# Kernel optimization log

Hardware: AMD Instinct MI355X
Metric: run time of the kernel (lower is better)

The kernel has to match this reference:

```python
import jax, jax.numpy as jnp
import numpy as np


def setup_inputs() -> dict:
    key = jax.random.key(0)
    k1, k2, k3 = jax.random.split(key, 3)
    B, S, E = 4, 4096, 512
    x = jax.random.normal(k1, (B, S, E), dtype=jnp.float32)
    # xavier_uniform for Linear weights; zero biases (per _reset_parameters)
    lim_qkv = float(np.sqrt(6.0 / (E + 3 * E)))
    W_qkv = jax.random.uniform(k2, (3 * E, E), minval=-lim_qkv, maxval=lim_qkv, dtype=jnp.float32)
    b_qkv = jnp.zeros((3 * E,), dtype=jnp.float32)
    lim_out = float(np.sqrt(6.0 / (E + E)))
    W_out = jax.random.uniform(k3, (E, E), minval=-lim_out, maxval=lim_out, dtype=jnp.float32)
    b_out = jnp.zeros((E,), dtype=jnp.float32)
    return {"x": x, "W_qkv": W_qkv, "b_qkv": b_qkv, "W_out": W_out, "b_out": b_out}


def reference(x, W_qkv, b_qkv, W_out, b_out):
    B, S, E = x.shape
    H = 8
    D = E // H
    qkv = x @ W_qkv.T + b_qkv                      # [B,S,3E]
    qkv = qkv.reshape(B, S, H, 3 * D)
    q, k, v = jnp.split(qkv, 3, axis=-1)            # each [B,S,H,D]
    q = jax.nn.sigmoid(q)
    k = jax.nn.sigmoid(k)
    # flow conservation normalizers (sum over seq dim=1, then feature dim=3)
    i = jnp.sum(q * jnp.sum(k, axis=1, keepdims=True), axis=3, keepdims=True)      # [B,S,H,1]
    o = jnp.sum(k * jnp.sum(q, axis=1, keepdims=True), axis=3, keepdims=True)
    i_hat = jnp.sum(q * jnp.sum(k / o, axis=1, keepdims=True), axis=3, keepdims=True)
    o_hat = jnp.sum(k * jnp.sum(q / i, axis=1, keepdims=True), axis=3, keepdims=True)
    # NOTE: faithful to source — matmul batches over (B,S) and contracts the HEAD axis
    vw = v * jax.nn.softmax(o_hat, axis=1)          # [B,S,H,D]
    kv = jnp.einsum('bshd,bshe->bsde', k, vw)       # [B,S,D,D]
    r = jnp.einsum('bshd,bsde->bshe', q / i, kv) * jax.nn.sigmoid(i_hat)  # [B,S,H,D]
    values = r.reshape(B, S, E)
    return values @ W_out.T + b_out
```

## Files before the change

kernel.cpp:

```cpp
#include <hip/hip_runtime.h>
#include <cstdint>
#include <cstddef>

#define B_ 4
#define S_ 4096
#define E_ 512
#define NPOS 16384
#define QKVC 1536
#define K_ 512

typedef unsigned short u16;
typedef u16    u16x8  __attribute__((ext_vector_type(8)));
typedef u16    u16x4  __attribute__((ext_vector_type(4)));
typedef __bf16 bf16x8 __attribute__((ext_vector_type(8)));
typedef float  f32x4  __attribute__((ext_vector_type(4)));

__device__ __forceinline__ u16 f2bf(float f) {
    unsigned u = __builtin_bit_cast(unsigned, f);
    unsigned r = (u + 0x7fffu + ((u >> 16) & 1u)) >> 16;
    return (u16)r;
}
__device__ __forceinline__ float bf2f(u16 u) {
    return __builtin_bit_cast(float, (unsigned)u << 16);
}
__device__ __forceinline__ float rcpf(float x) { return __builtin_amdgcn_rcpf(x); }

__device__ __forceinline__ void async16(const void* g, void* lds) {
    __builtin_amdgcn_global_load_lds(
        (const __attribute__((address_space(1))) unsigned int*)g,
        (__attribute__((address_space(3))) unsigned int*)lds, 16, 0, 0);
}

__global__ void cvt_kernel(const float4* __restrict__ in, u16x4* __restrict__ out, int n4) {
    int i = blockIdx.x * 256 + threadIdx.x;
    if (i < n4) {
        float4 v = in[i];
        u16x4 o;
        o[0] = f2bf(v.x); o[1] = f2bf(v.y); o[2] = f2bf(v.z); o[3] = f2bf(v.w);
        out[i] = o;
    }
}

__device__ __forceinline__ void mfma_step(const u16* AsB, const u16* BsB,
                                          int wm, int wn, int fr, int fkk,
                                          f32x4 (&acc)[4][4]) {
    bf16x8 a[4], b[4];
    #pragma unroll
    for (int i = 0; i < 4; ++i)
        a[i] = *(const bf16x8*)&AsB[(wm + i * 16 + fr) * 32 + fkk];
    #pragma unroll
    for (int j = 0; j < 4; ++j)
        b[j] = *(const bf16x8*)&BsB[(wn + j * 16 + fr) * 32 + fkk];
    __builtin_amdgcn_s_setprio(1);
    #pragma unroll
    for (int i = 0; i < 4; ++i)
        #pragma unroll
        for (int j = 0; j < 4; ++j)
            acc[i][j] = __builtin_amdgcn_mfma_f32_16x16x32_bf16(a[i], b[j], acc[i][j], 0, 0, 0);
    __builtin_amdgcn_s_setprio(0);
}

#define GEMM_PIPELINE(NT)                                                     \
    {                                                                          \
        STAGE(0, 0);                                                           \
        STAGE(1, 1);                                                           \
        asm volatile("s_waitcnt vmcnt(4)" ::: "memory");                       \
        __builtin_amdgcn_s_barrier();                                          \
        __builtin_amdgcn_sched_barrier(0);                                     \
        int cb = 0, sb = 1;                                                    \
        for (int t = 0; t < (NT) - 2; ++t) {                                   \
            sb = (sb == 2) ? 0 : sb + 1;                                       \
            STAGE(t + 2, sb);                                                  \
            mfma_step(As[cb], Bs[cb], wm, wn, fr, fkk, acc);                   \
            asm volatile("s_waitcnt vmcnt(4)" ::: "memory");                   \
            __builtin_amdgcn_s_barrier();                                      \
            __builtin_amdgcn_sched_barrier(0);                                 \
            cb = (cb == 2) ? 0 : cb + 1;                                       \
        }                                                                      \
        mfma_step(As[cb], Bs[cb], wm, wn, fr, fkk, acc);                       \
        asm volatile("s_waitcnt vmcnt(0)" ::: "memory");                       \
        __builtin_amdgcn_s_barrier();                                          \
        __builtin_amdgcn_sched_barrier(0);                                     \
        cb = (cb == 2) ? 0 : cb + 1;                                           \
        mfma_step(As[cb], Bs[cb], wm, wn, fr, fkk, acc);                       \
    }

__global__ __launch_bounds__(256) void gemm_qkv(
        const u16* __restrict__ A, const u16* __restrict__ Bw,
        const float* __restrict__ bias,
        u16* __restrict__ Qb, u16* __restrict__ Kb, u16* __restrict__ Vb,
        float* __restrict__ sumq, float* __restrict__ sumk,
        int K) {
    __shared__ u16 As[3][128 * 32];
    __shared__ u16 Bs[3][128 * 32];
    const int tid  = threadIdx.x;
    const int wave = tid >> 6, lane = tid & 63;
    const int bid = blockIdx.x;
    const int swz = (bid & 7) * 192 + (bid >> 3);
    const int m0 = (swz / 12) * 128, n0 = (swz % 12) * 128;
    const int wm = (wave & 1) * 64, wn = (wave >> 1) * 64;

    const int srow = wave * 16 + (lane >> 2);
    const int cgs  = (lane & 3) ^ ((lane >> 2) & 3) ^ ((lane >> 4) & 3);
    const u16* Ap = A  + (size_t)(m0 + srow) * K + cgs * 8;
    const u16* Bp = Bw + (size_t)(n0 + srow) * K + cgs * 8;
    const int woff = wave * 512;
    const size_t rstep = (size_t)64 * K;

    f32x4 acc[4][4] = {};
    const int fr  = lane & 15;
    const int fkk = (((lane >> 4) ^ (fr & 3) ^ ((fr >> 2) & 3))) * 8;

    #define STAGE(t, buf)                                             \
        async16(Ap + (t) * 32,         &As[buf][woff]);               \
        async16(Ap + (t) * 32 + rstep, &As[buf][woff + 2048]);        \
        async16(Bp + (t) * 32,         &Bs[buf][woff]);               \
        async16(Bp + (t) * 32 + rstep, &Bs[buf][woff + 2048]);

    const int nt = K >> 5;
    GEMM_PIPELINE(nt)
    #undef STAGE

    const int cn = lane & 15, rb = (lane >> 4) * 4;
    const int cg   = (n0 + wn) >> 6;
    const int type = cg % 3;
    const int hb   = cg / 3;
    u16* dst = (type == 0) ? Qb : (type == 1) ? Kb : Vb;
    const bool sg = (type < 2);
    float colsum[4] = {};
    #pragma unroll
    for (int i = 0; i < 4; ++i) {
        int mbase = m0 + wm + i * 16 + rb;
        #pragma unroll
        for (int j = 0; j < 4; ++j) {
            int ccol = j * 16 + cn;
            float bv = bias[n0 + wn + ccol];
            int outcol = hb * 64 + ccol;
            f32x4 av = acc[i][j];
            #pragma unroll
            for (int r = 0; r < 4; ++r) {
                float v = av[r] + bv;
                if (sg) { v = 1.f / (1.f + __expf(-v)); colsum[j] += v; }
                dst[(size_t)(mbase + r) * 512 + outcol] = f2bf(v);
            }
        }
    }
    if (sg) {
        float* sdst = (type == 0) ? sumq : sumk;
        const int b = m0 >> 12;
        #pragma unroll
        for (int j = 0; j < 4; ++j) {
            float s = colsum[j];
            s += __shfl_xor(s, 16);
            s += __shfl_xor(s, 32);
            if (lane < 16)
                atomicAdd(&sdst[b * 512 + hb * 64 + j * 16 + cn], s);
        }
    }
}

__global__ __launch_bounds__(256) void gemm_out(
        const u16* __restrict__ A, const u16* __restrict__ Bw,
        const float* __restrict__ bias, float* __restrict__ C,
        int N, int K) {
    __shared__ u16 As[3][128 * 32];
    __shared__ u16 Bs[3][128 * 32];
    const int tid  = threadIdx.x;
    const int wave = tid >> 6, lane = tid & 63;
    const int bid = blockIdx.x;
    const int swz = (bid & 7) * 64 + (bid >> 3);
    const int m0 = (swz >> 2) * 128, n0 = (swz & 3) * 128;
    const int wm = (wave & 1) * 64, wn = (wave >> 1) * 64;
    const int srow = wave * 16 + (lane >> 2);
    const int cgs  = (lane & 3) ^ ((lane >> 2) & 3) ^ ((lane >> 4) & 3);
    const u16* Ap = A  + (size_t)(m0 + srow) * K + cgs * 8;
    const u16* Bp = Bw + (size_t)(n0 + srow) * K + cgs * 8;
    const int woff = wave * 512;
    const size_t rstep = (size_t)64 * K;
    f32x4 acc[4][4] = {};
    const int fr  = lane & 15;
    const int fkk = (((lane >> 4) ^ (fr & 3) ^ ((fr >> 2) & 3))) * 8;

    #define STAGE(t, buf)                                             \
        async16(Ap + (t) * 32,         &As[buf][woff]);               \
        async16(Ap + (t) * 32 + rstep, &As[buf][woff + 2048]);        \
        async16(Bp + (t) * 32,         &Bs[buf][woff]);               \
        async16(Bp + (t) * 32 + rstep, &Bs[buf][woff + 2048]);

    const int nt = K >> 5;
    GEMM_PIPELINE(nt)
    #undef STAGE

    const int cn = lane & 15, rb = (lane >> 4) * 4;
    #pragma unroll
    for (int i = 0; i < 4; ++i) {
        int mbase = m0 + wm + i * 16 + rb;
        #pragma unroll
        for (int j = 0; j < 4; ++j) {
            int nn = n0 + wn + j * 16 + cn;
            float bv = bias[nn];
            f32x4 av = acc[i][j];
            #pragma unroll
            for (int r = 0; r < 4; ++r)
                C[(size_t)(mbase + r) * N + nn] = av[r] + bv;
        }
    }
}

__global__ __launch_bounds__(256) void fused_io(const u16* __restrict__ Qg, const u16* __restrict__ Kg,
                                                const float* __restrict__ sumq, const float* __restrict__ sumk,
                                                float* __restrict__ iv,
                                                float* __restrict__ sumqi, float* __restrict__ sumko) {
    int b = blockIdx.x, sc = blockIdx.y;
    int w = threadIdx.x >> 6, lane = threadIdx.x & 63;
    float skL[8], sqL[8];
    #pragma unroll
    for (int j = 0; j < 8; ++j) {
        skL[j] = sumk[b * 512 + lane * 8 + j];
        sqL[j] = sumq[b * 512 + lane * 8 + j];
    }
    float aqi[8] = {}, ako[8] = {};
    int p0 = b * S_ + sc * 32 + w * 8;
    for (int it = 0; it < 8; ++it) {
        int p = p0 + it;
        size_t off = (size_t)p * 512 + lane * 8;
        u16x8 q8 = *(const u16x8*)(Qg + off);
        u16x8 k8 = *(const u16x8*)(Kg + off);
        float qf[8], kf[8];
        #pragma unroll
        for (int j = 0; j < 8; ++j) { qf[j] = bf2f(q8[j]); kf[j] = bf2f(k8[j]); }
        float di = 0.f, dox = 0.f;
        #pragma unroll
        for (int j = 0; j < 8; ++j) { di += qf[j] * skL[j]; dox += kf[j] * sqL[j]; }
        di  += __shfl_xor(di, 1);  di  += __shfl_xor(di, 2);  di  += __shfl_xor(di, 4);
        dox += __shfl_xor(dox, 1); dox += __shfl_xor(dox, 2); dox += __shfl_xor(dox, 4);
        if ((lane & 7) == 0) iv[(size_t)p * 8 + (lane >> 3)] = di;
        float ri = rcpf(di), ro = rcpf(dox);
        #pragma unroll
        for (int j = 0; j < 8; ++j) { aqi[j] += qf[j] * ri; ako[j] += kf[j] * ro; }
    }
    __shared__ float red[4][1024];
    #pragma unroll
    for (int j = 0; j < 8; ++j) {
        red[w][lane * 8 + j]       = aqi[j];
        red[w][512 + lane * 8 + j] = ako[j];
    }
    __syncthreads();
    int t = threadIdx.x;
    #pragma unroll
    for (int rr = 0; rr < 4; ++rr) {
        int slot = rr * 256 + t;
        float s = red[0][slot] + red[1][slot] + red[2][slot] + red[3][slot];
        float* dst = (slot < 512) ? &sumqi[b * 512 + slot] : &sumko[b * 512 + (slot - 512)];
        atomicAdd(dst, s);
    }
}

__global__ __launch_bounds__(256) void io2_kernel(const u16* __restrict__ Qg, const u16* __restrict__ Kg,
                                                  const float* __restrict__ sumqi, const float* __restrict__ sumko,
                                                  const float* __restrict__ iv,
                                                  float* __restrict__ rowsc, float* __restrict__ wexp,
                                                  float* __restrict__ sm) {
    int b = blockIdx.x, sc = blockIdx.y;
    int w = threadIdx.x >> 6, lane = threadIdx.x & 63;
    float skoL[8], sqiL[8];
    #pragma unroll
    for (int j = 0; j < 8; ++j) {
        skoL[j] = sumko[b * 512 + lane * 8 + j];
        sqiL[j] = sumqi[b * 512 + lane * 8 + j];
    }
    float smacc = 0.f;
    int p0 = b * S_ + sc * 32 + w * 8;
    for (int it = 0; it < 8; ++it) {
        int p = p0 + it;
        size_t off = (size_t)p * 512 + lane * 8;
        u16x8 q8 = *(const u16x8*)(Qg + off);
        u16x8 k8 = *(const u16x8*)(Kg + off);
        float dih = 0.f, doh = 0.f;
        #pragma unroll
        for (int j = 0; j < 8; ++j) {
            dih += bf2f(q8[j]) * skoL[j];
            doh += bf2f(k8[j]) * sqiL[j];
        }
        dih += __shfl_xor(dih, 1); dih += __shfl_xor(dih, 2); dih += __shfl_xor(dih, 4);
        doh += __shfl_xor(doh, 1); doh += __shfl_xor(doh, 2); doh += __shfl_xor(doh, 4);
        if ((lane & 7) == 0) {
            int h = lane >> 3;
            float sig = 1.f / (1.f + __expf(-dih));
            rowsc[(size_t)p * 8 + h] = sig * rcpf(iv[(size_t)p * 8 + h]);
            float we = __expf(fminf(doh, 80.f));
            wexp[(size_t)p * 8 + h] = we;
            smacc += we;
        }
    }
    __shared__ float sr[4][8];
    if ((lane & 7) == 0) sr[w][lane >> 3] = smacc;
    __syncthreads();
    if (threadIdx.x < 8)
        atomicAdd(&sm[b * 8 + threadIdx.x],
                  sr[0][threadIdx.x] + sr[1][threadIdx.x] + sr[2][threadIdx.x] + sr[3][threadIdx.x]);
}

__global__ __launch_bounds__(256) void finalize_kernel(
        const u16* __restrict__ Qg, const u16* __restrict__ Kg, const u16* __restrict__ Vg,
        const float* __restrict__ rowsc, const float* __restrict__ wexp, const float* __restrict__ sm,
        u16* __restrict__ Rg) {
    __shared__ float Ml[4][2][8][9];
    __shared__ float vw[4][2][8][68];
    int w = threadIdx.x >> 6, lane = threadIdx.x & 63;
    int p0 = (blockIdx.x * 4 + w) * 2;
    int b = p0 >> 12;

    {
        int pl = (lane >> 3) & 1, hh = lane & 7, quad = lane >> 4;
        const u16* qa = Qg + (size_t)(p0 + pl) * 512 + hh * 64 + quad * 8;
        const u16* ka = Kg + (size_t)(p0 + pl) * 512 + hh * 64 + quad * 8;
        bf16x8 a0 = __builtin_bit_cast(bf16x8, *(const u16x8*)qa);
        bf16x8 a1 = __builtin_bit_cast(bf16x8, *(const u16x8*)(qa + 32));
        bf16x8 b0 = __builtin_bit_cast(bf16x8, *(const u16x8*)ka);
        bf16x8 b1 = __builtin_bit_cast(bf16x8, *(const u16x8*)(ka + 32));
        f32x4 accm = {0.f, 0.f, 0.f, 0.f};
        accm = __builtin_amdgcn_mfma_f32_16x16x32_bf16(a0, b0, accm, 0, 0, 0);
        accm = __builtin_amdgcn_mfma_f32_16x16x32_bf16(a1, b1, accm, 0, 0, 0);
        if (((lane >> 5) & 1) == ((lane >> 3) & 1)) {
            int plm = lane >> 5, hr = ((lane >> 4) & 1) * 4, h2 = lane & 7;
            #pragma unroll
            for (int r = 0; r < 4; ++r) Ml[w][plm][hr + r][h2] = accm[r];
        }
    }
    {
        int hv = lane >> 3, e0 = (lane & 7) * 8;
        float invsm = rcpf(sm[b * 8 + hv]);
        #pragma unroll
        for (int pl = 0; pl < 2; ++pl) {
            u16x8 v8 = *(const u16x8*)(Vg + (size_t)(p0 + pl) * 512 + lane * 8);
            float wgt = wexp[(size_t)(p0 + pl) * 8 + hv] * invsm;
            f32x4 x0, x1;
            #pragma unroll
            for (int j = 0; j < 4; ++j) { x0[j] = bf2f(v8[j]) * wgt; x1[j] = bf2f(v8[4 + j]) * wgt; }
            *(f32x4*)&vw[w][pl][hv][e0]     = x0;
            *(f32x4*)&vw[w][pl][hv][e0 + 4] = x1;
        }
    }
    __syncthreads();
    {
        int pl = lane >> 5, idx = lane & 31, h = idx >> 2, eq = (idx & 3) * 16;
        float out[16] = {};
        #pragma unroll
        for (int h2 = 0; h2 < 8; ++h2) {
            float m = Ml[w][pl][h][h2];
            #pragma unroll
            for (int c = 0; c < 4; ++c) {
                f32x4 vv = *(const f32x4*)&vw[w][pl][h2][eq + c * 4];
                #pragma unroll
                for (int j = 0; j < 4; ++j) out[c * 4 + j] += m * vv[j];
            }
        }
        float rs = rowsc[(size_t)(p0 + pl) * 8 + h];
        u16x8 o0, o1;
        #pragma unroll
        for (int j = 0; j < 8; ++j) { o0[j] = f2bf(out[j] * rs); o1[j] = f2bf(out[8 + j] * rs); }
        u16* dst = Rg + (size_t)(p0 + pl) * 512 + h * 64 + eq;
        *(u16x8*)dst       = o0;
        *(u16x8*)(dst + 8) = o1;
    }
}

extern "C" void kernel_launch(void* const* d_in, const int* in_sizes, int n_in,
                              void* d_out, int out_size, void* d_ws, size_t ws_size,
                              hipStream_t stream) {
    const float* x    = (const float*)d_in[0];
    const float* Wqkv = (const float*)d_in[1];
    const float* bqkv = (const float*)d_in[2];
    const float* Wout = (const float*)d_in[3];
    const float* bout = (const float*)d_in[4];
    float* out = (float*)d_out;
    char* ws = (char*)d_ws;

    constexpr size_t SZ_XBF  = (size_t)NPOS * E_ * 2;
    constexpr size_t SZ_WQBF = (size_t)QKVC * E_ * 2;
    constexpr size_t SZ_WOBF = (size_t)E_ * E_ * 2;
    constexpr size_t SZ_QKVB = (size_t)NPOS * E_ * 2;
    constexpr size_t SZ_SUM  = (size_t)B_ * 512 * 4;
    constexpr size_t SZ_V8   = (size_t)NPOS * 8 * 4;

    size_t off = 0;
    u16*   xbf   = (u16*)(ws + off);   off += SZ_XBF;
    u16*   wqbf  = (u16*)(ws + off);   off += SZ_WQBF;
    u16*   wobf  = (u16*)(ws + off);   off += SZ_WOBF;
    u16*   Qb    = (u16*)(ws + off);   off += SZ_QKVB;
    u16*   Kb    = (u16*)(ws + off);   off += SZ_QKVB;
    u16*   Vb    = (u16*)(ws + off);   off += SZ_QKVB;
    char*  zbase = ws + off;
    float* sumq  = (float*)(ws + off); off += SZ_SUM;
    float* sumk  = (float*)(ws + off); off += SZ_SUM;
    float* sumqi = (float*)(ws + off); off += SZ_SUM;
    float* sumko = (float*)(ws + off); off += SZ_SUM;
    float* sm    = (float*)(ws + off); off += 256;
    size_t zlen  = (char*)(ws + off) - zbase;
    float* iv    = (float*)(ws + off); off += SZ_V8;
    float* rowsc = (float*)(ws + off); off += SZ_V8;
    float* wexp  = (float*)(ws + off); off += SZ_V8;
    u16*   rbf   = xbf;

    hipMemsetAsync(zbase, 0, zlen, stream);

    cvt_kernel<<<(NPOS * E_ / 4) / 256, 256, 0, stream>>>((const float4*)x, (u16x4*)xbf, NPOS * E_ / 4);
    cvt_kernel<<<(QKVC * E_ / 4) / 256, 256, 0, stream>>>((const float4*)Wqkv, (u16x4*)wqbf, QKVC * E_ / 4);
    cvt_kernel<<<(E_ * E_ / 4) / 256, 256, 0, stream>>>((const float4*)Wout, (u16x4*)wobf, E_ * E_ / 4);

    gemm_qkv<<<dim3((QKVC / 128) * (NPOS / 128)), 256, 0, stream>>>(xbf, wqbf, bqkv, Qb, Kb, Vb, sumq, sumk, K_);

    fused_io<<<dim3(B_, 128), 256, 0, stream>>>(Qb, Kb, sumq, sumk, iv, sumqi, sumko);
    io2_kernel<<<dim3(B_, 128), 256, 0, stream>>>(Qb, Kb, sumqi, sumko, iv, rowsc, wexp, sm);
    finalize_kernel<<<NPOS / 8, 256, 0, stream>>>(Qb, Kb, Vb, rowsc, wexp, sm, rbf);

    gemm_out<<<dim3((E_ / 128) * (NPOS / 128)), 256, 0, stream>>>(rbf, wobf, bout, out, E_, K_);
}
```

Measured before the change: 186.3 us.

## Fuse flow-normalizer kernels into one cooperative kernel with LDS-resident Q/K

```diff
diff --git a/kernel.cpp b/kernel.cpp
--- a/kernel.cpp
+++ b/kernel.cpp
@@ -1,6 +1,9 @@
 #include <hip/hip_runtime.h>
+#include <hip/hip_cooperative_groups.h>
 #include <cstdint>
 #include <cstddef>
+
+namespace cg = cooperative_groups;
 
 #define B_ 4
 #define S_ 4096
@@ -31,14 +34,21 @@
         (__attribute__((address_space(3))) unsigned int*)lds, 16, 0, 0);
 }
 
-__global__ void cvt_kernel(const float4* __restrict__ in, u16x4* __restrict__ out, int n4) {
+#define CVT_N1 (NPOS * E_ / 4)
+#define CVT_N2 (QKVC * E_ / 4)
+#define CVT_N3 (E_ * E_ / 4)
+__global__ void cvt_all(const float4* __restrict__ x,  u16x4* __restrict__ xo,
+                        const float4* __restrict__ wq, u16x4* __restrict__ wqo,
+                        const float4* __restrict__ wo, u16x4* __restrict__ woo) {
     int i = blockIdx.x * 256 + threadIdx.x;
-    if (i < n4) {
-        float4 v = in[i];
-        u16x4 o;
-        o[0] = f2bf(v.x); o[1] = f2bf(v.y); o[2] = f2bf(v.z); o[3] = f2bf(v.w);
-        out[i] = o;
-    }
+    const float4* in; u16x4* out; int idx;
+    if (i < CVT_N1)                { in = x;  out = xo;  idx = i; }
+    else if (i < CVT_N1 + CVT_N2)  { in = wq; out = wqo; idx = i - CVT_N1; }
+    else                           { in = wo; out = woo; idx = i - CVT_N1 - CVT_N2; }
+    float4 v = in[idx];
+    u16x4 o;
+    o[0] = f2bf(v.x); o[1] = f2bf(v.y); o[2] = f2bf(v.z); o[3] = f2bf(v.w);
+    out[idx] = o;
 }
 
 __device__ __forceinline__ void mfma_step(const u16* AsB, const u16* BsB,
@@ -122,9 +132,9 @@
     #undef STAGE
 
     const int cn = lane & 15, rb = (lane >> 4) * 4;
-    const int cg   = (n0 + wn) >> 6;
-    const int type = cg % 3;
-    const int hb   = cg / 3;
+    const int cg2  = (n0 + wn) >> 6;
+    const int type = cg2 % 3;
+    const int hb   = cg2 / 3;
     u16* dst = (type == 0) ? Qb : (type == 1) ? Kb : Vb;
     const bool sg = (type < 2);
     float colsum[4] = {};
@@ -207,162 +217,178 @@
     }
 }
 
-__global__ __launch_bounds__(256) void fused_io(const u16* __restrict__ Qg, const u16* __restrict__ Kg,
-                                                const float* __restrict__ sumq, const float* __restrict__ sumk,
-                                                float* __restrict__ iv,
-                                                float* __restrict__ sumqi, float* __restrict__ sumko) {
-    int b = blockIdx.x, sc = blockIdx.y;
-    int w = threadIdx.x >> 6, lane = threadIdx.x & 63;
-    float skL[8], sqL[8];
-    #pragma unroll
-    for (int j = 0; j < 8; ++j) {
-        skL[j] = sumk[b * 512 + lane * 8 + j];
-        sqL[j] = sumq[b * 512 + lane * 8 + j];
-    }
-    float aqi[8] = {}, ako[8] = {};
-    int p0 = b * S_ + sc * 32 + w * 8;
-    for (int it = 0; it < 8; ++it) {
-        int p = p0 + it;
-        size_t off = (size_t)p * 512 + lane * 8;
-        u16x8 q8 = *(const u16x8*)(Qg + off);
-        u16x8 k8 = *(const u16x8*)(Kg + off);
-        float qf[8], kf[8];
-        #pragma unroll
-        for (int j = 0; j < 8; ++j) { qf[j] = bf2f(q8[j]); kf[j] = bf2f(k8[j]); }
-        float di = 0.f, dox = 0.f;
-        #pragma unroll
-        for (int j = 0; j < 8; ++j) { di += qf[j] * skL[j]; dox += kf[j] * sqL[j]; }
-        di  += __shfl_xor(di, 1);  di  += __shfl_xor(di, 2);  di  += __shfl_xor(di, 4);
-        dox += __shfl_xor(dox, 1); dox += __shfl_xor(dox, 2); dox += __shfl_xor(dox, 4);
-        if ((lane & 7) == 0) iv[(size_t)p * 8 + (lane >> 3)] = di;
-        float ri = rcpf(di), ro = rcpf(dox);
-        #pragma unroll
-        for (int j = 0; j < 8; ++j) { aqi[j] += qf[j] * ri; ako[j] += kf[j] * ro; }
-    }
-    __shared__ float red[4][1024];
-    #pragma unroll
-    for (int j = 0; j < 8; ++j) {
-        red[w][lane * 8 + j]       = aqi[j];
-        red[w][512 + lane * 8 + j] = ako[j];
-    }
-    __syncthreads();
-    int t = threadIdx.x;
-    #pragma unroll
-    for (int rr = 0; rr < 4; ++rr) {
-        int slot = rr * 256 + t;
-        float s = red[0][slot] + red[1][slot] + red[2][slot] + red[3][slot];
-        float* dst = (slot < 512) ? &sumqi[b * 512 + slot] : &sumko[b * 512 + (slot - 512)];
-        atomicAdd(dst, s);
-    }
-}
-
-__global__ __launch_bounds__(256) void io2_kernel(const u16* __restrict__ Qg, const u16* __restrict__ Kg,
-                                                  const float* __restrict__ sumqi, const float* __restrict__ sumko,
-                                                  const float* __restrict__ iv,
-                                                  float* __restrict__ rowsc, float* __restrict__ wexp,
-                                                  float* __restrict__ sm) {
-    int b = blockIdx.x, sc = blockIdx.y;
-    int w = threadIdx.x >> 6, lane = threadIdx.x & 63;
-    float skoL[8], sqiL[8];
-    #pragma unroll
-    for (int j = 0; j < 8; ++j) {
-        skoL[j] = sumko[b * 512 + lane * 8 + j];
-        sqiL[j] = sumqi[b * 512 + lane * 8 + j];
-    }
-    float smacc = 0.f;
-    int p0 = b * S_ + sc * 32 + w * 8;
-    for (int it = 0; it < 8; ++it) {
-        int p = p0 + it;
-        size_t off = (size_t)p * 512 + lane * 8;
-        u16x8 q8 = *(const u16x8*)(Qg + off);
-        u16x8 k8 = *(const u16x8*)(Kg + off);
-        float dih = 0.f, doh = 0.f;
+__global__ __launch_bounds__(256) void coopflow(
+        const u16* __restrict__ Qg, const u16* __restrict__ Kg, const u16* __restrict__ Vg,
+        const float* __restrict__ sumq, const float* __restrict__ sumk,
+        float* __restrict__ sumqi, float* __restrict__ sumko, float* __restrict__ sm,
+        u16* __restrict__ Rg) {
+    __shared__ u16 Qs[64 * 512];
+    __shared__ u16 Ks[64 * 512];
+    __shared__ float scratch[4928];
+    __shared__ float iv_l[64][8];
+    __shared__ float rowsc_l[64][8];
+    __shared__ float wexp_l[64][8];
+    __shared__ float sr[4][8];
+
+    const int bid = blockIdx.x;
+    const int b   = bid >> 6;
+    const int P0  = b * S_ + (bid & 63) * 64;
+    const int w = threadIdx.x >> 6, lane = threadIdx.x & 63;
+
+    {
+        float* red = scratch;
+        float skL[8], sqL[8];
         #pragma unroll
         for (int j = 0; j < 8; ++j) {
-            dih += bf2f(q8[j]) * skoL[j];
-            doh += bf2f(k8[j]) * sqiL[j];
-        }
-        dih += __shfl_xor(dih, 1); dih += __shfl_xor(dih, 2); dih += __shfl_xor(dih, 4);
-        doh += __shfl_xor(doh, 1); doh += __shfl_xor(doh, 2); doh += __shfl_xor(doh, 4);
-        if ((lane & 7) == 0) {
-            int h = lane >> 3;
-            float sig = 1.f / (1.f + __expf(-dih));
-            rowsc[(size_t)p * 8 + h] = sig * rcpf(iv[(size_t)p * 8 + h]);
-            float we = __expf(fminf(doh, 80.f));
-            wexp[(size_t)p * 8 + h] = we;
-            smacc += we;
-        }
-    }
-    __shared__ float sr[4][8];
-    if ((lane & 7) == 0) sr[w][lane >> 3] = smacc;
-    __syncthreads();
-    if (threadIdx.x < 8)
-        atomicAdd(&sm[b * 8 + threadIdx.x],
-                  sr[0][threadIdx.x] + sr[1][threadIdx.x] + sr[2][threadIdx.x] + sr[3][threadIdx.x]);
-}
-
-__global__ __launch_bounds__(256) void finalize_kernel(
-        const u16* __restrict__ Qg, const u16* __restrict__ Kg, const u16* __restrict__ Vg,
-        const float* __restrict__ rowsc, const float* __restrict__ wexp, const float* __restrict__ sm,
-        u16* __restrict__ Rg) {
-    __shared__ float Ml[4][2][8][9];
-    __shared__ float vw[4][2][8][68];
-    int w = threadIdx.x >> 6, lane = threadIdx.x & 63;
-    int p0 = (blockIdx.x * 4 + w) * 2;
-    int b = p0 >> 12;
+            skL[j] = sumk[b * 512 + lane * 8 + j];
+            sqL[j] = sumq[b * 512 + lane * 8 + j];
+        }
+        for (int half = 0; half < 2; ++half) {
+            float aqi[8] = {}, ako[8] = {};
+            int pl0 = half * 32 + w * 8;
+            for (int it = 0; it < 8; ++it) {
+                int pll = pl0 + it;
+                size_t off = (size_t)(P0 + pll) * 512 + lane * 8;
+                u16x8 q8 = *(const u16x8*)(Qg + off);
+                u16x8 k8 = *(const u16x8*)(Kg + off);
+                *(u16x8*)&Qs[pll * 512 + lane * 8] = q8;
+                *(u16x8*)&Ks[pll * 512 + lane * 8] = k8;
+                float qf[8], kf[8];
+                #pragma unroll
+                for (int j = 0; j < 8; ++j) { qf[j] = bf2f(q8[j]); kf[j] = bf2f(k8[j]); }
+                float di = 0.f, dox = 0.f;
+                #pragma unroll
+                for (int j = 0; j < 8; ++j) { di += qf[j] * skL[j]; dox += kf[j] * sqL[j]; }
+                di  += __shfl_xor(di, 1);  di  += __shfl_xor(di, 2);  di  += __shfl_xor(di, 4);
+                dox += __shfl_xor(dox, 1); dox += __shfl_xor(dox, 2); dox += __shfl_xor(dox, 4);
+                if ((lane & 7) == 0) iv_l[pll][lane >> 3] = di;
+                float ri = rcpf(di), ro = rcpf(dox);
+                #pragma unroll
+                for (int j = 0; j < 8; ++j) { aqi[j] += qf[j] * ri; ako[j] += kf[j] * ro; }
+            }
+            #pragma unroll
+            for (int j = 0; j < 8; ++j) {
+                red[w * 1024 + lane * 8 + j]       = aqi[j];
+                red[w * 1024 + 512 + lane * 8 + j] = ako[j];
+            }
+            __syncthreads();
+            int t = threadIdx.x;
+            #pragma unroll
+            for (int rr = 0; rr < 4; ++rr) {
+                int slot = rr * 256 + t;
+                float s = red[slot] + red[1024 + slot] + red[2048 + slot] + red[3072 + slot];
+                float* dst = (slot < 512) ? &sumqi[b * 512 + slot] : &sumko[b * 512 + (slot - 512)];
+                atomicAdd(dst, s);
+            }
+            __syncthreads();
+        }
+    }
+    cg::this_grid().sync();
 
     {
-        int pl = (lane >> 3) & 1, hh = lane & 7, quad = lane >> 4;
-        const u16* qa = Qg + (size_t)(p0 + pl) * 512 + hh * 64 + quad * 8;
-        const u16* ka = Kg + (size_t)(p0 + pl) * 512 + hh * 64 + quad * 8;
-        bf16x8 a0 = __builtin_bit_cast(bf16x8, *(const u16x8*)qa);
-        bf16x8 a1 = __builtin_bit_cast(bf16x8, *(const u16x8*)(qa + 32));
-        bf16x8 b0 = __builtin_bit_cast(bf16x8, *(const u16x8*)ka);
-        bf16x8 b1 = __builtin_bit_cast(bf16x8, *(const u16x8*)(ka + 32));
-        f32x4 accm = {0.f, 0.f, 0.f, 0.f};
-        accm = __builtin_amdgcn_mfma_f32_16x16x32_bf16(a0, b0, accm, 0, 0, 0);
-        accm = __builtin_amdgcn_mfma_f32_16x16x32_bf16(a1, b1, accm, 0, 0, 0);
-        if (((lane >> 5) & 1) == ((lane >> 3) & 1)) {
-            int plm = lane >> 5, hr = ((lane >> 4) & 1) * 4, h2 = lane & 7;
-            #pragma unroll
-            for (int r = 0; r < 4; ++r) Ml[w][plm][hr + r][h2] = accm[r];
-        }
-    }
+        float skoL[8], sqiL[8];
+        #pragma unroll
+        for (int j = 0; j < 8; ++j) {
+            skoL[j] = sumko[b * 512 + lane * 8 + j];
+            sqiL[j] = sumqi[b * 512 + lane * 8 + j];
+        }
+        for (int half = 0; half < 2; ++half) {
+            float smacc = 0.f;
+            int pl0 = half * 32 + w * 8;
+            for (int it = 0; it < 8; ++it) {
+                int pll = pl0 + it;
+                u16x8 q8 = *(const u16x8*)&Qs[pll * 512 + lane * 8];
+                u16x8 k8 = *(const u16x8*)&Ks[pll * 512 + lane * 8];
+                float dih = 0.f, doh = 0.f;
+                #pragma unroll
+                for (int j = 0; j < 8; ++j) {
+                    dih += bf2f(q8[j]) * skoL[j];
+                    doh += bf2f(k8[j]) * sqiL[j];
+                }
+                dih += __shfl_xor(dih, 1); dih += __shfl_xor(dih, 2); dih += __shfl_xor(dih, 4);
+                doh += __shfl_xor(doh, 1); doh += __shfl_xor(doh, 2); doh += __shfl_xor(doh, 4);
+                if ((lane & 7) == 0) {
+                    int h = lane >> 3;
+                    float sig = 1.f / (1.f + __expf(-dih));
+                    rowsc_l[pll][h] = sig * rcpf(iv_l[pll][h]);
+                    float we = __expf(fminf(doh, 80.f));
+                    wexp_l[pll][h] = we;
+                    smacc += we;
+                }
+            }
+            if ((lane & 7) == 0) sr[w][lane >> 3] = smacc;
+            __syncthreads();
+            if (threadIdx.x < 8)
+                atomicAdd(&sm[b * 8 + threadIdx.x],
+                          sr[0][threadIdx.x] + sr[1][threadIdx.x] + sr[2][threadIdx.x] + sr[3][threadIdx.x]);
+            __syncthreads();
+        }
+    }
+    cg::this_grid().sync();
+
     {
-        int hv = lane >> 3, e0 = (lane & 7) * 8;
-        float invsm = rcpf(sm[b * 8 + hv]);
-        #pragma unroll
-        for (int pl = 0; pl < 2; ++pl) {
-            u16x8 v8 = *(const u16x8*)(Vg + (size_t)(p0 + pl) * 512 + lane * 8);
-            float wgt = wexp[(size_t)(p0 + pl) * 8 + hv] * invsm;
-            f32x4 x0, x1;
-            #pragma unroll
-            for (int j = 0; j < 4; ++j) { x0[j] = bf2f(v8[j]) * wgt; x1[j] = bf2f(v8[4 + j]) * wgt; }
-            *(f32x4*)&vw[w][pl][hv][e0]     = x0;
-            *(f32x4*)&vw[w][pl][hv][e0 + 4] = x1;
-        }
-    }
-    __syncthreads();
-    {
-        int pl = lane >> 5, idx = lane & 31, h = idx >> 2, eq = (idx & 3) * 16;
-        float out[16] = {};
-        #pragma unroll
-        for (int h2 = 0; h2 < 8; ++h2) {
-            float m = Ml[w][pl][h][h2];
-            #pragma unroll
-            for (int c = 0; c < 4; ++c) {
-                f32x4 vv = *(const f32x4*)&vw[w][pl][h2][eq + c * 4];
-                #pragma unroll
-                for (int j = 0; j < 4; ++j) out[c * 4 + j] += m * vv[j];
-            }
-        }
-        float rs = rowsc[(size_t)(p0 + pl) * 8 + h];
-        u16x8 o0, o1;
-        #pragma unroll
-        for (int j = 0; j < 8; ++j) { o0[j] = f2bf(out[j] * rs); o1[j] = f2bf(out[8 + j] * rs); }
-        u16* dst = Rg + (size_t)(p0 + pl) * 512 + h * 64 + eq;
-        *(u16x8*)dst       = o0;
-        *(u16x8*)(dst + 8) = o1;
+        float* Ml = scratch;
+        float* vw = scratch + 576;
+        const float invsm = rcpf(sm[b * 8 + (lane >> 3)]);
+        __syncthreads();
+        for (int g = 0; g < 8; ++g) {
+            const int ploc = g * 8 + w * 2;
+            const int p0g  = P0 + ploc;
+            {
+                int pl = (lane >> 3) & 1, hh = lane & 7, quad = lane >> 4;
+                const u16* qa = &Qs[(ploc + pl) * 512 + hh * 64 + quad * 8];
+                const u16* ka = &Ks[(ploc + pl) * 512 + hh * 64 + quad * 8];
+                bf16x8 a0 = __builtin_bit_cast(bf16x8, *(const u16x8*)qa);
+                bf16x8 a1 = __builtin_bit_cast(bf16x8, *(const u16x8*)(qa + 32));
+                bf16x8 b0 = __builtin_bit_cast(bf16x8, *(const u16x8*)ka);
+                bf16x8 b1 = __builtin_bit_cast(bf16x8, *(const u16x8*)(ka + 32));
+                f32x4 accm = {0.f, 0.f, 0.f, 0.f};
+                accm = __builtin_amdgcn_mfma_f32_16x16x32_bf16(a0, b0, accm, 0, 0, 0);
+                accm = __builtin_amdgcn_mfma_f32_16x16x32_bf16(a1, b1, accm, 0, 0, 0);
+                if (((lane >> 5) & 1) == ((lane >> 3) & 1)) {
+                    int plm = lane >> 5, hr = ((lane >> 4) & 1) * 4, h2 = lane & 7;
+                    #pragma unroll
+                    for (int r = 0; r < 4; ++r)
+                        Ml[w * 144 + plm * 72 + (hr + r) * 9 + h2] = accm[r];
+                }
+            }
+            {
+                int hv = lane >> 3, e0 = (lane & 7) * 8;
+                #pragma unroll
+                for (int pl = 0; pl < 2; ++pl) {
+                    u16x8 v8 = *(const u16x8*)(Vg + (size_t)(p0g + pl) * 512 + lane * 8);
+                    float wgt = wexp_l[ploc + pl][hv] * invsm;
+                    f32x4 x0, x1;
+                    #pragma unroll
+                    for (int j = 0; j < 4; ++j) { x0[j] = bf2f(v8[j]) * wgt; x1[j] = bf2f(v8[4 + j]) * wgt; }
+                    *(f32x4*)&vw[w * 1088 + pl * 544 + hv * 68 + e0]     = x0;
+                    *(f32x4*)&vw[w * 1088 + pl * 544 + hv * 68 + e0 + 4] = x1;
+                }
+            }
+            __syncthreads();
+            {
+                int pl = lane >> 5, idx = lane & 31, h = idx >> 2, eq = (idx & 3) * 16;
+                float out[16] = {};
+                #pragma unroll
+                for (int h2 = 0; h2 < 8; ++h2) {
+                    float m = Ml[w * 144 + pl * 72 + h * 9 + h2];
+                    #pragma unroll
+                    for (int c = 0; c < 4; ++c) {
+                        f32x4 vv = *(const f32x4*)&vw[w * 1088 + pl * 544 + h2 * 68 + eq + c * 4];
+                        #pragma unroll
+                        for (int j = 0; j < 4; ++j) out[c * 4 + j] += m * vv[j];
+                    }
+                }
+                float rs = rowsc_l[ploc + pl][h];
+                u16x8 o0, o1;
+                #pragma unroll
+                for (int j = 0; j < 8; ++j) { o0[j] = f2bf(out[j] * rs); o1[j] = f2bf(out[8 + j] * rs); }
+                u16* dst = Rg + (size_t)(p0g + pl) * 512 + h * 64 + eq;
+                *(u16x8*)dst       = o0;
+                *(u16x8*)(dst + 8) = o1;
+            }
+            __syncthreads();
+        }
     }
 }
 
@@ -382,7 +408,6 @@
     constexpr size_t SZ_WOBF = (size_t)E_ * E_ * 2;
     constexpr size_t SZ_QKVB = (size_t)NPOS * E_ * 2;
     constexpr size_t SZ_SUM  = (size_t)B_ * 512 * 4;
-    constexpr size_t SZ_V8   = (size_t)NPOS * 8 * 4;
 
     size_t off = 0;
     u16*   xbf   = (u16*)(ws + off);   off += SZ_XBF;
@@ -398,22 +423,25 @@
     float* sumko = (float*)(ws + off); off += SZ_SUM;
     float* sm    = (float*)(ws + off); off += 256;
     size_t zlen  = (char*)(ws + off) - zbase;
-    float* iv    = (float*)(ws + off); off += SZ_V8;
-    float* rowsc = (float*)(ws + off); off += SZ_V8;
-    float* wexp  = (float*)(ws + off); off += SZ_V8;
     u16*   rbf   = xbf;
 
     hipMemsetAsync(zbase, 0, zlen, stream);
 
-    cvt_kernel<<<(NPOS * E_ / 4) / 256, 256, 0, stream>>>((const float4*)x, (u16x4*)xbf, NPOS * E_ / 4);
-    cvt_kernel<<<(QKVC * E_ / 4) / 256, 256, 0, stream>>>((const float4*)Wqkv, (u16x4*)wqbf, QKVC * E_ / 4);
-    cvt_kernel<<<(E_ * E_ / 4) / 256, 256, 0, stream>>>((const float4*)Wout, (u16x4*)wobf, E_ * E_ / 4);
+    cvt_all<<<(CVT_N1 + CVT_N2 + CVT_N3) / 256, 256, 0, stream>>>(
+        (const float4*)x, (u16x4*)xbf,
+        (const float4*)Wqkv, (u16x4*)wqbf,
+        (const float4*)Wout, (u16x4*)wobf);
 
     gemm_qkv<<<dim3((QKVC / 128) * (NPOS / 128)), 256, 0, stream>>>(xbf, wqbf, bqkv, Qb, Kb, Vb, sumq, sumk, K_);
 
-    fused_io<<<dim3(B_, 128), 256, 0, stream>>>(Qb, Kb, sumq, sumk, iv, sumqi, sumko);
-    io2_kernel<<<dim3(B_, 128), 256, 0, stream>>>(Qb, Kb, sumqi, sumko, iv, rowsc, wexp, sm);
-    finalize_kernel<<<NPOS / 8, 256, 0, stream>>>(Qb, Kb, Vb, rowsc, wexp, sm, rbf);
+    {
+        const u16* Qa = Qb; const u16* Ka = Kb; const u16* Va = Vb;
+        void* cargs[] = {(void*)&Qa, (void*)&Ka, (void*)&Va,
+                         (void*)&sumq, (void*)&sumk,
+                         (void*)&sumqi, (void*)&sumko, (void*)&sm,
+                         (void*)&rbf};
+        hipLaunchCooperativeKernel((const void*)coopflow, dim3(256), dim3(256), cargs, 0, stream);
+    }
 
     gemm_out<<<dim3((E_ / 128) * (NPOS / 128)), 256, 0, stream>>>(rbf, wobf, bout, out, E_, K_);
 }
```

After: 244.3 us. 1.31x slower.
